# Kernel optimization log

Hardware: AMD Instinct MI355X
Metric: run time of the kernel (lower is better)

## Reference

```python
import jax, jax.numpy as jnp
import numpy as np

D_MODEL, D_K, D_V, N_HEADS = 1024, 64, 64, 16
B, S = 4, 4096
LN_EPS = 1e-5
NORM_EPS = 1e-12  # torch F.normalize default eps


def setup_inputs() -> dict:
    key = jax.random.key(0)
    ks = jax.random.split(key, 9)
    s = 0.02
    return {
        "x": jax.random.normal(ks[0], (B, S, D_MODEL), dtype=jnp.float32),
        # nn.Linear weights have shape [out, in]
        "W_Q": jax.random.normal(ks[1], (N_HEADS * D_K, D_MODEL), dtype=jnp.float32) * s,
        "W_K": jax.random.normal(ks[2], (N_HEADS * D_K, D_MODEL), dtype=jnp.float32) * s,
        "W_V": jax.random.normal(ks[3], (N_HEADS * D_V, D_MODEL), dtype=jnp.float32) * s,
        "W_g": jax.random.normal(ks[4], (N_HEADS * D_V, D_MODEL), dtype=jnp.float32) * s,
        "W_alpha": jax.random.normal(ks[5], (N_HEADS, D_MODEL), dtype=jnp.float32) * s,
        "W_O": jax.random.normal(ks[6], (D_MODEL, N_HEADS * D_V), dtype=jnp.float32) * s,
        "ln_gamma": jnp.ones((D_MODEL,), dtype=jnp.float32),
        "ln_beta": jnp.zeros((D_MODEL,), dtype=jnp.float32),
    }


def reference(x, W_Q, W_K, W_V, W_g, W_alpha, W_O, ln_gamma, ln_beta):
    # --- input projection chain (unfused variant) ---
    Q_raw = jnp.einsum('bsd,od->bso', x, W_Q)               # [B,S,H*Dk] (unused downstream)
    K_raw = jnp.einsum('bsd,od->bso', x, W_K)               # [B,S,H*Dk]
    V = jnp.einsum('bsd,od->bso', x, W_V)                   # [B,S,H*Dv]
    g_raw = jnp.einsum('bsd,od->bso', x, W_g)               # [B,S,H*Dv]
    alpha_raw = jnp.einsum('bsd,od->bso', x, W_alpha)       # [B,S,H]

    # F.normalize over the full last dim (n_heads*d_k), eps clamp on the norm
    K_norm = K_raw / jnp.maximum(jnp.linalg.norm(K_raw, axis=-1, keepdims=True), NORM_EPS)
    gate = jax.nn.silu(g_raw)
    alpha = jax.nn.sigmoid(alpha_raw)

    # scan is simulated as identity: scan_output = V
    scan_output = V

    # --- output epilogue: gate-multiply + output GEMM + residual + LayerNorm ---
    gated = scan_output * gate
    projected = jnp.einsum('bsv,dv->bsd', gated, W_O)
    pre = projected + x
    mean = jnp.mean(pre, axis=-1, keepdims=True)
    var = jnp.mean(jnp.square(pre - mean), axis=-1, keepdims=True)
    out = (pre - mean) * jax.lax.rsqrt(var + LN_EPS) * ln_gamma + ln_beta
    return out
```

## Files before the change

### kernel.cpp

```cpp
#include <hip/hip_runtime.h>

#define M_TOT 16384
#define DM    1024

typedef unsigned short ushort_t;
typedef __bf16 bf16x8 __attribute__((ext_vector_type(8)));
typedef float  f32x4  __attribute__((ext_vector_type(4)));

__device__ __forceinline__ ushort_t f32_to_bf16(float f) {
    union { float f; unsigned u; } v; v.f = f;
    unsigned u = v.u;
    return (ushort_t)((u + 0x7fffu + ((u >> 16) & 1u)) >> 16);
}
__device__ __forceinline__ float bf16_to_f32(ushort_t h) {
    union { unsigned u; float f; } v; v.u = ((unsigned)h) << 16;
    return v.f;
}

__device__ __forceinline__ void gload16(const ushort_t* g, ushort_t* l) {
    __builtin_amdgcn_global_load_lds(
        (const __attribute__((address_space(1))) unsigned int*)g,
        (__attribute__((address_space(3))) unsigned int*)l,
        16, 0, 0);
}

__global__ __launch_bounds__(256) void cvt_all(const float* __restrict__ x,
                                               const float* __restrict__ wv,
                                               const float* __restrict__ wg,
                                               const float* __restrict__ wo,
                                               ushort_t* __restrict__ xkt,
                                               ushort_t* __restrict__ wcat,
                                               ushort_t* __restrict__ wob) {
    const long NX = (long)M_TOT * DM / 4, NW = (long)DM * DM / 4;
    long i = (long)blockIdx.x * 256 + threadIdx.x;
    const float* src; ushort_t* dst; long so, di;
    if (i < NX) {
        src = x; so = i;
        int row = (int)(i >> 8), col0 = (int)(i & 255) << 2;
        dst = xkt;
        di = ((long)(col0 >> 5) * M_TOT + row) * 8 + ((col0 & 31) >> 2);
    } else if (i < NX + NW) {
        long j = i - NX; src = wv; so = j;
        int row = (int)(j >> 8), col0 = (int)(j & 255) << 2;
        int orow = ((row >> 4) << 5) | (row & 15);
        dst = wcat;
        di = ((long)(col0 >> 5) * 2048 + orow) * 8 + ((col0 & 31) >> 2);
    } else if (i < NX + 2 * NW) {
        long j = i - NX - NW; src = wg; so = j;
        int row = (int)(j >> 8), col0 = (int)(j & 255) << 2;
        int orow = ((row >> 4) << 5) | 16 | (row & 15);
        dst = wcat;
        di = ((long)(col0 >> 5) * 2048 + orow) * 8 + ((col0 & 31) >> 2);
    } else {
        long j = i - NX - 2 * NW; src = wo; so = j;
        int row = (int)(j >> 8), col0 = (int)(j & 255) << 2;
        dst = wob;
        di = ((long)(col0 >> 5) * 1024 + row) * 8 + ((col0 & 31) >> 2);
    }
    const float4 v = ((const float4*)src)[so];
    ushort4 o;
    o.x = f32_to_bf16(v.x); o.y = f32_to_bf16(v.y);
    o.z = f32_to_bf16(v.z); o.w = f32_to_bf16(v.w);
    ((ushort4*)dst)[di] = o;
}

template<int EPI, int NB>
__global__ __launch_bounds__(512, 2) void gemmS(
    const ushort_t* __restrict__ A,
    const ushort_t* __restrict__ Bm,
    const ushort_t* __restrict__ Xb,
    ushort_t* __restrict__ out0,
    int nbs)
{
    extern __shared__ ushort_t lds[];

    const int flat = blockIdx.x;
    const int xcd  = flat & 7;
    const int ii   = flat >> 3;
    const int m0   = ((xcd << 3) + (ii >> nbs)) << 8;
    const int n0   = (ii & ((1 << nbs) - 1)) << 8;

    const int tid  = threadIdx.x;
    const int w    = tid >> 6;
    const int l    = tid & 63;
    const int wm   = w >> 2;
    const int wn   = w & 3;
    const int fr   = l & 15;
    const int quad = l >> 4;

    f32x4 acc[8][4];
    const f32x4 vzero = {0.f, 0.f, 0.f, 0.f};
#pragma unroll
    for (int i = 0; i < 8; ++i)
#pragma unroll
        for (int j = 0; j < 4; ++j) acc[i][j] = vzero;

    const int sA = (m0 + w * 16 + fr) * 32 + (quad << 3);
    const int sB = (n0 + w * 16 + fr) * 32 + (quad << 3);

    auto stageA = [&](int u) {
        const int  d  = (u & 3) * 16384 + w * 512;
        const long po = (long)u * (M_TOT * 32);
        gload16(A + po + sA, lds + d);
        gload16(A + po + sA + 4096, lds + d + 4096);
    };
    auto stageB = [&](int u) {
        const int  d  = (u & 3) * 16384 + 8192 + w * 512;
        const long po = (long)u * (NB * 32);
        gload16(Bm + po + sB, lds + d);
        gload16(Bm + po + sB + 4096, lds + d + 4096);
    };

    const int rA = wm * 4096 + l * 8;
    const int rB = 8192 + wn * 2048 + l * 8;

    stageA(0); stageB(0);
    stageA(1); stageB(1);
    stageA(2); stageB(2);
    asm volatile("s_waitcnt vmcnt(8)" ::: "memory");
    __builtin_amdgcn_s_barrier();

    for (int u = 0; u < 32; ++u) {
        const int sb = (u & 3) * 16384;
        bf16x8 af[4], bf[4];

#pragma unroll
        for (int j = 0; j < 4; ++j) bf[j] = *(const bf16x8*)(lds + sb + rB + j * 512);
#pragma unroll
        for (int i = 0; i < 4; ++i) af[i] = *(const bf16x8*)(lds + sb + rA + i * 512);
        if (u < 29) stageA(u + 3);
        __builtin_amdgcn_s_barrier();
        __builtin_amdgcn_s_setprio(1);
#pragma unroll
        for (int j = 0; j < 4; ++j)
#pragma unroll
            for (int i = 0; i < 4; ++i)
                acc[i][j] = __builtin_amdgcn_mfma_f32_16x16x32_bf16(
                    af[i], bf[j], acc[i][j], 0, 0, 0);
        __builtin_amdgcn_s_setprio(0);
        __builtin_amdgcn_s_barrier();

#pragma unroll
        for (int i = 0; i < 4; ++i) af[i] = *(const bf16x8*)(lds + sb + rA + (4 + i) * 512);
        if (u < 29) stageB(u + 3);
        __builtin_amdgcn_s_barrier();
        __builtin_amdgcn_s_setprio(1);
#pragma unroll
        for (int j = 0; j < 4; ++j)
#pragma unroll
            for (int i = 0; i < 4; ++i)
                acc[4 + i][j] = __builtin_amdgcn_mfma_f32_16x16x32_bf16(
                    af[i], bf[j], acc[4 + i][j], 0, 0, 0);
        __builtin_amdgcn_s_setprio(0);
        if (u < 29)       { asm volatile("s_waitcnt vmcnt(8)" ::: "memory"); }
        else if (u == 29) { asm volatile("s_waitcnt vmcnt(4)" ::: "memory"); }
        else if (u == 30) { asm volatile("s_waitcnt vmcnt(0)" ::: "memory"); }
        __builtin_amdgcn_sched_barrier(0);
        __builtin_amdgcn_s_barrier();
    }

    const int rowb = m0 + wm * 128;
    const int colb = n0 + wn * 64;
    if (EPI == 0) {
#pragma unroll
        for (int i = 0; i < 8; ++i)
#pragma unroll
            for (int jp = 0; jp < 2; ++jp) {
                const int cb   = colb + jp * 32;
                const int vcol = ((cb >> 5) << 4) + fr;
                const long kbase = ((long)(vcol >> 5) * M_TOT) * 32 + (vcol & 31);
#pragma unroll
                for (int r = 0; r < 4; ++r) {
                    const int row = rowb + i * 16 + quad * 4 + r;
                    float v = acc[i][2 * jp][r];
                    float g = acc[i][2 * jp + 1][r];
                    float gate = g / (1.0f + __expf(-g));
                    out0[kbase + (long)row * 32] = f32_to_bf16(v * gate);
                }
            }
    } else {
#pragma unroll
        for (int i = 0; i < 8; ++i)
#pragma unroll
            for (int j = 0; j < 4; ++j) {
                const int col = colb + j * 16 + fr;
                const long xbase = ((long)(col >> 5) * M_TOT) * 32 + (col & 31);
#pragma unroll
                for (int r = 0; r < 4; ++r) {
                    const int row = rowb + i * 16 + quad * 4 + r;
                    float pre = acc[i][j][r] + bf16_to_f32(Xb[xbase + (long)row * 32]);
                    out0[(long)row * DM + col] = f32_to_bf16(pre);
                }
            }
    }
}

__global__ __launch_bounds__(256) void ln_rows(const ushort_t* __restrict__ pre,
                                               const float* __restrict__ gamma,
                                               const float* __restrict__ beta,
                                               float* __restrict__ out)
{
    const int row = blockIdx.x;
    const int tid = threadIdx.x;
    const int wave = tid >> 6, lane = tid & 63;

    ushort4 u = ((const ushort4*)(pre + (long)row * DM))[tid];
    float p0 = bf16_to_f32(u.x), p1 = bf16_to_f32(u.y);
    float p2 = bf16_to_f32(u.z), p3 = bf16_to_f32(u.w);

    float s  = p0 + p1 + p2 + p3;
    float ss = p0 * p0 + p1 * p1 + p2 * p2 + p3 * p3;
#pragma unroll
    for (int off = 32; off > 0; off >>= 1) {
        s  += __shfl_down(s, off);
        ss += __shfl_down(ss, off);
    }
    __shared__ float red[8];
    __shared__ float mb[2];
    if (lane == 0) { red[wave] = s; red[4 + wave] = ss; }
    __syncthreads();
    if (tid == 0) {
        float S  = red[0] + red[1] + red[2] + red[3];
        float SS = red[4] + red[5] + red[6] + red[7];
        float mean = S * (1.0f / 1024.0f);
        float var  = SS * (1.0f / 1024.0f) - mean * mean;
        mb[0] = mean;
        mb[1] = rsqrtf(var + 1e-5f);
    }
    __syncthreads();
    const float mean = mb[0], rs = mb[1];

    float4 gm = ((const float4*)gamma)[tid];
    float4 bt = ((const float4*)beta)[tid];
    float4 o;
    o.x = (p0 - mean) * rs * gm.x + bt.x;
    o.y = (p1 - mean) * rs * gm.y + bt.y;
    o.z = (p2 - mean) * rs * gm.z + bt.z;
    o.w = (p3 - mean) * rs * gm.w + bt.w;
    ((float4*)(out + (long)row * DM))[tid] = o;
}

extern "C" void kernel_launch(void* const* d_in, const int* in_sizes, int n_in,
                              void* d_out, int out_size, void* d_ws, size_t ws_size,
                              hipStream_t stream) {
    const float* x     = (const float*)d_in[0];
    const float* WV    = (const float*)d_in[3];
    const float* WG    = (const float*)d_in[4];
    const float* WO    = (const float*)d_in[6];
    const float* gamma = (const float*)d_in[7];
    const float* beta  = (const float*)d_in[8];
    float* out = (float*)d_out;

    const size_t SZX = (size_t)M_TOT * DM * 2;
    const size_t SZW = (size_t)DM * DM * 2;
    char* ws = (char*)d_ws;
    ushort_t* xkt   = (ushort_t*)ws;
    ushort_t* gated = (ushort_t*)(ws + SZX);
    ushort_t* wcat  = (ushort_t*)(ws + 2 * SZX);
    ushort_t* wob   = (ushort_t*)(ws + 2 * SZX + 2 * SZW);
    ushort_t* pre   = (ushort_t*)(ws + 2 * SZX + 3 * SZW);

    static bool attr_set = false;
    if (!attr_set) {
        hipFuncSetAttribute((const void*)&gemmS<0, 2048>,
                            hipFuncAttributeMaxDynamicSharedMemorySize, 131072);
        hipFuncSetAttribute((const void*)&gemmS<1, 1024>,
                            hipFuncAttributeMaxDynamicSharedMemorySize, 131072);
        attr_set = true;
    }

    const int nCvt = (M_TOT * DM + 3 * DM * DM) / 4 / 256;
    cvt_all<<<nCvt, 256, 0, stream>>>(x, WV, WG, WO, xkt, wcat, wob);

    gemmS<0, 2048><<<512, 512, 131072, stream>>>(xkt, wcat, nullptr, gated, 3);
    gemmS<1, 1024><<<256, 512, 131072, stream>>>(gated, wob, xkt, pre, 2);

    ln_rows<<<M_TOT, 256, 0, stream>>>(pre, gamma, beta, out);
}
```

Before: 269.5 us.

## Stage GEMM epilogues through swizzled LDS for coalesced stores; move residual to LN

New measurement: 292.0 us. 1.08x slower.

```diff
diff --git a/kernel.cpp b/kernel.cpp
--- a/kernel.cpp
+++ b/kernel.cpp
@@ -31,44 +31,51 @@
                                                ushort_t* __restrict__ xkt,
                                                ushort_t* __restrict__ wcat,
                                                ushort_t* __restrict__ wob) {
-    const long NX = (long)M_TOT * DM / 4, NW = (long)DM * DM / 4;
-    long i = (long)blockIdx.x * 256 + threadIdx.x;
-    const float* src; ushort_t* dst; long so, di;
-    if (i < NX) {
-        src = x; so = i;
-        int row = (int)(i >> 8), col0 = (int)(i & 255) << 2;
-        dst = xkt;
-        di = ((long)(col0 >> 5) * M_TOT + row) * 8 + ((col0 & 31) >> 2);
-    } else if (i < NX + NW) {
-        long j = i - NX; src = wv; so = j;
-        int row = (int)(j >> 8), col0 = (int)(j & 255) << 2;
-        int orow = ((row >> 4) << 5) | (row & 15);
+    const long CX = (long)M_TOT * DM / 8;
+    const long CW = (long)2 * DM * DM / 8;
+    long t = (long)blockIdx.x * 256 + threadIdx.x;
+    const float* src; ushort_t* dst; long soff, doff;
+    if (t < CX) {
+        long q = t;
+        int c = (int)(q & 3);
+        int row = (int)((q >> 2) & (M_TOT - 1));
+        int plane = (int)(q >> 16);
+        soff = (long)row * DM + plane * 32 + c * 8;
+        doff = ((long)plane * M_TOT + row) * 32 + c * 8;
+        src = x; dst = xkt;
+    } else if (t < CX + CW) {
+        long q = t - CX;
+        int c = (int)(q & 3);
+        int orow = (int)((q >> 2) & 2047);
+        int plane = (int)(q >> 13);
+        int srow = ((orow >> 5) << 4) | (orow & 15);
+        src = (orow & 16) ? wg : wv;
+        soff = (long)srow * DM + plane * 32 + c * 8;
+        doff = ((long)plane * 2048 + orow) * 32 + c * 8;
         dst = wcat;
-        di = ((long)(col0 >> 5) * 2048 + orow) * 8 + ((col0 & 31) >> 2);
-    } else if (i < NX + 2 * NW) {
-        long j = i - NX - NW; src = wg; so = j;
-        int row = (int)(j >> 8), col0 = (int)(j & 255) << 2;
-        int orow = ((row >> 4) << 5) | 16 | (row & 15);
-        dst = wcat;
-        di = ((long)(col0 >> 5) * 2048 + orow) * 8 + ((col0 & 31) >> 2);
     } else {
-        long j = i - NX - 2 * NW; src = wo; so = j;
-        int row = (int)(j >> 8), col0 = (int)(j & 255) << 2;
-        dst = wob;
-        di = ((long)(col0 >> 5) * 1024 + row) * 8 + ((col0 & 31) >> 2);
-    }
-    const float4 v = ((const float4*)src)[so];
-    ushort4 o;
-    o.x = f32_to_bf16(v.x); o.y = f32_to_bf16(v.y);
-    o.z = f32_to_bf16(v.z); o.w = f32_to_bf16(v.w);
-    ((ushort4*)dst)[di] = o;
+        long q = t - CX - CW;
+        int c = (int)(q & 3);
+        int row = (int)((q >> 2) & 1023);
+        int plane = (int)(q >> 12);
+        soff = (long)row * DM + plane * 32 + c * 8;
+        doff = ((long)plane * DM + row) * 32 + c * 8;
+        src = wo; dst = wob;
+    }
+    const float4 a = *(const float4*)(src + soff);
+    const float4 b = *(const float4*)(src + soff + 4);
+    union { ushort_t u[8]; int4 v; } o;
+    o.u[0] = f32_to_bf16(a.x); o.u[1] = f32_to_bf16(a.y);
+    o.u[2] = f32_to_bf16(a.z); o.u[3] = f32_to_bf16(a.w);
+    o.u[4] = f32_to_bf16(b.x); o.u[5] = f32_to_bf16(b.y);
+    o.u[6] = f32_to_bf16(b.z); o.u[7] = f32_to_bf16(b.w);
+    *(int4*)(dst + doff) = o.v;
 }
 
 template<int EPI, int NB>
 __global__ __launch_bounds__(512, 2) void gemmS(
     const ushort_t* __restrict__ A,
     const ushort_t* __restrict__ Bm,
-    const ushort_t* __restrict__ Xb,
     ushort_t* __restrict__ out0,
     int nbs)
 {
@@ -159,54 +166,94 @@
         __builtin_amdgcn_s_barrier();
     }
 
-    const int rowb = m0 + wm * 128;
-    const int colb = n0 + wn * 64;
     if (EPI == 0) {
+        ushort_t* bb = lds;
 #pragma unroll
         for (int i = 0; i < 8; ++i)
 #pragma unroll
             for (int jp = 0; jp < 2; ++jp) {
-                const int cb   = colb + jp * 32;
-                const int vcol = ((cb >> 5) << 4) + fr;
-                const long kbase = ((long)(vcol >> 5) * M_TOT) * 32 + (vcol & 31);
+                const int colL = wn * 32 + jp * 16 + fr;
+                const int chB  = colL >> 3;
 #pragma unroll
                 for (int r = 0; r < 4; ++r) {
-                    const int row = rowb + i * 16 + quad * 4 + r;
+                    const int rowL = wm * 128 + i * 16 + quad * 4 + r;
+                    const int sw   = (chB & 8) | ((chB ^ rowL) & 7);
                     float v = acc[i][2 * jp][r];
                     float g = acc[i][2 * jp + 1][r];
                     float gate = g / (1.0f + __expf(-g));
-                    out0[kbase + (long)row * 32] = f32_to_bf16(v * gate);
+                    bb[rowL * 128 + sw * 8 + (colL & 7)] = f32_to_bf16(v * gate);
                 }
             }
+        __builtin_amdgcn_s_barrier();
+#pragma unroll
+        for (int s = 0; s < 2; ++s) {
+            const int p   = tid & 3;
+            const int row = (tid >> 2) + s * 128;
+            int4 t0[4];
+#pragma unroll
+            for (int k = 0; k < 4; ++k) {
+                const int ch = p * 4 + k;
+                const int sw = (ch & 8) | ((ch ^ row) & 7);
+                t0[k] = *(const int4*)(bb + row * 128 + sw * 8);
+            }
+            const long gb = ((long)((n0 >> 6) + p) * M_TOT + (m0 + row)) * 32;
+#pragma unroll
+            for (int k = 0; k < 4; ++k)
+                *(int4*)(out0 + gb + k * 8) = t0[k];
+        }
     } else {
+        ushort_t* bb = lds;
 #pragma unroll
         for (int i = 0; i < 8; ++i)
 #pragma unroll
             for (int j = 0; j < 4; ++j) {
-                const int col = colb + j * 16 + fr;
-                const long xbase = ((long)(col >> 5) * M_TOT) * 32 + (col & 31);
+                const int colL = wn * 64 + j * 16 + fr;
+                const int chB  = colL >> 3;
 #pragma unroll
                 for (int r = 0; r < 4; ++r) {
-                    const int row = rowb + i * 16 + quad * 4 + r;
-                    float pre = acc[i][j][r] + bf16_to_f32(Xb[xbase + (long)row * 32]);
-                    out0[(long)row * DM + col] = f32_to_bf16(pre);
+                    const int rowL = wm * 128 + i * 16 + quad * 4 + r;
+                    const int sw   = (chB & 24) | ((chB ^ rowL) & 7);
+                    bb[rowL * 256 + sw * 8 + (colL & 7)] = f32_to_bf16(acc[i][j][r]);
                 }
             }
-    }
-}
-
-__global__ __launch_bounds__(256) void ln_rows(const ushort_t* __restrict__ pre,
-                                               const float* __restrict__ gamma,
-                                               const float* __restrict__ beta,
-                                               float* __restrict__ out)
+        __builtin_amdgcn_s_barrier();
+#pragma unroll
+        for (int s = 0; s < 4; ++s) {
+            const int p   = tid & 7;
+            const int row = (tid >> 3) + s * 64;
+            int4 t0[4];
+#pragma unroll
+            for (int k = 0; k < 4; ++k) {
+                const int ch = p * 4 + k;
+                const int sw = (ch & 24) | ((ch ^ row) & 7);
+                t0[k] = *(const int4*)(bb + row * 256 + sw * 8);
+            }
+            const long po = (long)(m0 + row) * DM + n0 + p * 32;
+#pragma unroll
+            for (int k = 0; k < 4; ++k)
+                *(int4*)(out0 + po + k * 8) = t0[k];
+        }
+    }
+}
+
+__global__ __launch_bounds__(256) void ln_rows2(const ushort_t* __restrict__ proj,
+                                                const ushort_t* __restrict__ xkt,
+                                                const float* __restrict__ gamma,
+                                                const float* __restrict__ beta,
+                                                float* __restrict__ out)
 {
     const int row = blockIdx.x;
     const int tid = threadIdx.x;
     const int wave = tid >> 6, lane = tid & 63;
 
-    ushort4 u = ((const ushort4*)(pre + (long)row * DM))[tid];
-    float p0 = bf16_to_f32(u.x), p1 = bf16_to_f32(u.y);
-    float p2 = bf16_to_f32(u.z), p3 = bf16_to_f32(u.w);
+    ushort4 up = ((const ushort4*)(proj + (long)row * DM))[tid];
+    const long xo = ((long)(tid >> 3) * M_TOT + row) * 32 + (tid & 7) * 4;
+    ushort4 ux = *(const ushort4*)(xkt + xo);
+
+    float p0 = bf16_to_f32(up.x) + bf16_to_f32(ux.x);
+    float p1 = bf16_to_f32(up.y) + bf16_to_f32(ux.y);
+    float p2 = bf16_to_f32(up.z) + bf16_to_f32(ux.z);
+    float p3 = bf16_to_f32(up.w) + bf16_to_f32(ux.w);
 
     float s  = p0 + p1 + p2 + p3;
     float ss = p0 * p0 + p1 * p1 + p2 * p2 + p3 * p3;
@@ -258,7 +305,7 @@
     ushort_t* gated = (ushort_t*)(ws + SZX);
     ushort_t* wcat  = (ushort_t*)(ws + 2 * SZX);
     ushort_t* wob   = (ushort_t*)(ws + 2 * SZX + 2 * SZW);
-    ushort_t* pre   = (ushort_t*)(ws + 2 * SZX + 3 * SZW);
+    ushort_t* proj  = (ushort_t*)(ws + 2 * SZX + 3 * SZW);
 
     static bool attr_set = false;
     if (!attr_set) {
@@ -269,11 +316,10 @@
         attr_set = true;
     }
 
-    const int nCvt = (M_TOT * DM + 3 * DM * DM) / 4 / 256;
-    cvt_all<<<nCvt, 256, 0, stream>>>(x, WV, WG, WO, xkt, wcat, wob);
-
-    gemmS<0, 2048><<<512, 512, 131072, stream>>>(xkt, wcat, nullptr, gated, 3);
-    gemmS<1, 1024><<<256, 512, 131072, stream>>>(gated, wob, xkt, pre, 2);
-
-    ln_rows<<<M_TOT, 256, 0, stream>>>(pre, gamma, beta, out);
-}
+    cvt_all<<<9728, 256, 0, stream>>>(x, WV, WG, WO, xkt, wcat, wob);
+
+    gemmS<0, 2048><<<512, 512, 131072, stream>>>(xkt, wcat, gated, 3);
+    gemmS<1, 1024><<<256, 512, 131072, stream>>>(gated, wob, proj, 2);
+
+    ln_rows2<<<M_TOT, 256, 0, stream>>>(proj, xkt, gamma, beta, out);
+}
```
